# Kernel tuning notes

Measured on AMD Instinct MI355X. Metric: run time of the kernel, lower is better.

The kernel has to match this reference:

```python
import jax, jax.numpy as jnp
import numpy as np

N = 10000      # atoms
E = 64000      # edges (precomputed radius-graph edge list)
B = 128        # molecules in the batch
H = 600        # SCHNET_HIDDEN = num_filters
G = 50         # SCHNET_NUM_GAUSSIANS
L = 6          # SCHNET_NUM_INTERACTIONS
CUTOFF = 10.0  # SCHNET_CUTOFF
ZVOCAB = 100   # PyG SchNet Embedding(100, hidden)
LOG2 = float(np.log(2.0))


def ssp(x):
    # shifted softplus, PyG SchNet activation
    return jax.nn.softplus(x) - LOG2


def setup_inputs() -> dict:
    key = jax.random.key(0)
    ks = jax.random.split(key, 16)
    s_h = 1.0 / np.sqrt(H)
    s_g = 1.0 / np.sqrt(G)
    z = jax.random.randint(ks[0], (N,), 0, 87)
    pos = jax.random.uniform(ks[1], (N, 3), dtype=jnp.float32) * 5.0  # dists < cutoff
    batch = jnp.sort(jax.random.randint(ks[2], (N,), 0, B))
    edge_index = jax.random.randint(ks[3], (2, E), 0, N)
    return {
        'z': z, 'pos': pos, 'batch': batch, 'edge_index': edge_index,
        'emb': jax.random.normal(ks[4], (ZVOCAB, H), jnp.float32) * 0.1,
        'mlp_w1': jax.random.normal(ks[5], (L, G, H), jnp.float32) * s_g,
        'mlp_b1': jnp.zeros((L, H), jnp.float32),
        'mlp_w2': jax.random.normal(ks[6], (L, H, H), jnp.float32) * s_h,
        'mlp_b2': jnp.zeros((L, H), jnp.float32),
        'lin1_w': jax.random.normal(ks[7], (L, H, H), jnp.float32) * s_h,
        'lin2_w': jax.random.normal(ks[8], (L, H, H), jnp.float32) * s_h,
        'lin2_b': jnp.zeros((L, H), jnp.float32),
        'int_lin_w': jax.random.normal(ks[9], (L, H, H), jnp.float32) * s_h,
        'int_lin_b': jnp.zeros((L, H), jnp.float32),
        'pool_w': jax.random.normal(ks[10], (H, H), jnp.float32) * s_h,
        'pool_b': jnp.zeros((H,), jnp.float32),
    }


def reference(z, pos, batch, edge_index, emb,
              mlp_w1, mlp_b1, mlp_w2, mlp_b2,
              lin1_w, lin2_w, lin2_b, int_lin_w, int_lin_b,
              pool_w, pool_b):
    src, dst = edge_index[0], edge_index[1]  # message flows src -> dst
    # edge geometry
    diff = pos[src] - pos[dst]                       # [E,3]
    d = jnp.sqrt(jnp.sum(diff * diff, axis=-1) + 1e-12)  # [E]
    # Gaussian smearing
    offset = jnp.linspace(0.0, CUTOFF, G, dtype=jnp.float32)
    coeff = -0.5 / (offset[1] - offset[0]) ** 2
    rbf = jnp.exp(coeff * (d[:, None] - offset[None, :]) ** 2)  # [E,G]
    # cosine cutoff
    C = 0.5 * (jnp.cos(d * (np.pi / CUTOFF)) + 1.0)             # [E]

    h = emb[z]  # [N,H]
    for k in range(L):
        # per-edge continuous filter
        W = ssp(rbf @ mlp_w1[k] + mlp_b1[k]) @ mlp_w2[k] + mlp_b2[k]  # [E,H]
        W = W * C[:, None]
        # CFConv: project, gather, modulate, scatter-add
        xj = (h @ lin1_w[k])[src]                                     # [E,H]
        agg = jax.ops.segment_sum(xj * W, dst, num_segments=N)        # [N,H]
        x = agg @ lin2_w[k] + lin2_b[k]
        x = ssp(x) @ int_lin_w[k] + int_lin_b[k]
        h = h + x  # residual interaction update

    # per-graph mean pool (segment mean), empty graphs stay zero
    sums = jax.ops.segment_sum(h, batch, num_segments=B)              # [B,H]
    cnt = jax.ops.segment_sum(jnp.ones((h.shape[0],), h.dtype), batch, num_segments=B)
    pooled = sums / jnp.maximum(cnt, 1.0)[:, None]
    return pooled @ pool_w + pool_b
```

## Files before the change

kernel.cpp:

```cpp
#include <hip/hip_runtime.h>
#include <math.h>


#define N_ATOMS 10000
#define E_EDGES 64000
#define B_MOLS  128
#define H_DIM   600
#define HP      608
#define G_DIM   50
#define L_LAYERS 6
#define M_TAB   1024
#define DMAX    8.67f
#define LOG2C   0.69314718056f

#define TM 64
#define TN 64
#define TK 32

typedef __attribute__((ext_vector_type(8))) short bf16x8;
typedef __attribute__((ext_vector_type(4))) float f32x4;

__device__ __forceinline__ float sspf(float x) {
    return fmaxf(x, 0.0f) + log1pf(expf(-fabsf(x))) - LOG2C;
}
__device__ __forceinline__ short f2bf(float x) {
    unsigned u = __float_as_uint(x);
    unsigned r = (u + 0x7FFF + ((u >> 16) & 1)) >> 16;
    return (short)r;
}
__device__ __forceinline__ float bf2f(short h) {
    return __uint_as_float(((unsigned)(unsigned short)h) << 16);
}
__device__ __forceinline__ int packsplit(float x) {
    short hi = f2bf(x);
    short lo = f2bf(x - bf2f(hi));
    return ((int)hi << 16) | ((int)lo & 0xffff);
}
__device__ __forceinline__ float unpackf(int p) {
    float fh = __uint_as_float((unsigned)p & 0xffff0000u);
    float fl = __uint_as_float(((unsigned)p) << 16);
    return fh + fl;
}

__device__ __forceinline__ void unpack_perm(const int4& p0, const int4& p1,
                                            int4& hi, int4& lo)
{
    hi.x = (int)__builtin_amdgcn_perm((unsigned)p0.y, (unsigned)p0.x, 0x07060302u);
    hi.y = (int)__builtin_amdgcn_perm((unsigned)p0.w, (unsigned)p0.z, 0x07060302u);
    hi.z = (int)__builtin_amdgcn_perm((unsigned)p1.y, (unsigned)p1.x, 0x07060302u);
    hi.w = (int)__builtin_amdgcn_perm((unsigned)p1.w, (unsigned)p1.z, 0x07060302u);
    lo.x = (int)__builtin_amdgcn_perm((unsigned)p0.y, (unsigned)p0.x, 0x05040100u);
    lo.y = (int)__builtin_amdgcn_perm((unsigned)p0.w, (unsigned)p0.z, 0x05040100u);
    lo.z = (int)__builtin_amdgcn_perm((unsigned)p1.y, (unsigned)p1.x, 0x05040100u);
    lo.w = (int)__builtin_amdgcn_perm((unsigned)p1.w, (unsigned)p1.z, 0x05040100u);
}

template<bool BIAS, bool ACT, bool ACCUM>
__global__ __launch_bounds__(256, 6)
void gemm_mfma(const int* __restrict__ A, int lda,
               const short* __restrict__ Bh, const short* __restrict__ Bl, int ldb,
               const float* __restrict__ bias,
               int* __restrict__ outP,
               int Ma, int K, int Nc)
{
    const int NT = (Nc + TN - 1) / TN;
    const int f = blockIdx.x;
    const int xcd = f & 7, s = f >> 3;
    const int n0 = (s % NT) * TN;
    const int m0 = (xcd + 8 * (s / NT)) * TM;
    if (m0 >= Ma) return;

    __shared__ __align__(16) short As[2][2048];
    __shared__ __align__(16) short Bs[2][2048];

    const int tid = threadIdx.x;
    const int lane = tid & 63, wid = tid >> 6;
    const int wm = (wid >> 1) * 32, wn = (wid & 1) * 32;
    const int l15 = lane & 15, quad = lane >> 4;

    const int srow = wid * 16 + l15;
    const int skk  = quad << 3;
    const int widx = wid * 512 + lane * 8;

    const int gm = min(m0 + srow, Ma - 1);
    const int gn = min(n0 + srow, Nc - 1);
    const int*   aPtr  = A  + (size_t)gm * lda + skk;
    const short* bPtrH = Bh + (size_t)gn * ldb + skk;
    const short* bPtrL = Bl + (size_t)gn * ldb + skk;

    f32x4 acc[2][2];
    #pragma unroll
    for (int i = 0; i < 2; ++i)
        #pragma unroll
        for (int j = 0; j < 2; ++j)
            acc[i][j] = (f32x4){0.f, 0.f, 0.f, 0.f};

    int4 ra0, ra1;
    bf16x8 rbh, rbl;

    ra0 = *(const int4*)aPtr; ra1 = *(const int4*)(aPtr + 4);
    rbh = *(const bf16x8*)bPtrH;
    rbl = *(const bf16x8*)bPtrL;
    aPtr += TK; bPtrH += TK; bPtrL += TK;

    for (int k0 = 0; k0 < K; k0 += TK) {
        {
            int4 hi, lo;
            unpack_perm(ra0, ra1, hi, lo);
            *(int4*)&As[0][widx] = hi;
            *(int4*)&As[1][widx] = lo;
            *(bf16x8*)&Bs[0][widx] = rbh;
            *(bf16x8*)&Bs[1][widx] = rbl;
        }
        __syncthreads();

        if (k0 + TK < K) {
            ra0 = *(const int4*)aPtr; ra1 = *(const int4*)(aPtr + 4);
            rbh = *(const bf16x8*)bPtrH;
            rbl = *(const bf16x8*)bPtrL;
            aPtr += TK; bPtrH += TK; bPtrL += TK;
        }

        bf16x8 a_h[2], a_l[2], b_h[2], b_l[2];
        #pragma unroll
        for (int mi = 0; mi < 2; ++mi) {
            int ridx = ((wm >> 4) + mi) * 512 + lane * 8;
            a_h[mi] = *(const bf16x8*)&As[0][ridx];
            a_l[mi] = *(const bf16x8*)&As[1][ridx];
        }
        #pragma unroll
        for (int ni = 0; ni < 2; ++ni) {
            int ridx = ((wn >> 4) + ni) * 512 + lane * 8;
            b_h[ni] = *(const bf16x8*)&Bs[0][ridx];
            b_l[ni] = *(const bf16x8*)&Bs[1][ridx];
        }

        #pragma unroll
        for (int mi = 0; mi < 2; ++mi)
            #pragma unroll
            for (int ni = 0; ni < 2; ++ni) {
                acc[mi][ni] = __builtin_amdgcn_mfma_f32_16x16x32_bf16(
                    a_h[mi], b_h[ni], acc[mi][ni], 0, 0, 0);
                acc[mi][ni] = __builtin_amdgcn_mfma_f32_16x16x32_bf16(
                    a_h[mi], b_l[ni], acc[mi][ni], 0, 0, 0);
                acc[mi][ni] = __builtin_amdgcn_mfma_f32_16x16x32_bf16(
                    a_l[mi], b_h[ni], acc[mi][ni], 0, 0, 0);
            }
        __syncthreads();
    }

    #pragma unroll
    for (int mi = 0; mi < 2; ++mi) {
        #pragma unroll
        for (int r = 0; r < 4; ++r) {
            int row = m0 + wm + mi * 16 + quad * 4 + r;
            if (row >= Ma) continue;
            #pragma unroll
            for (int ni = 0; ni < 2; ++ni) {
                int col = n0 + wn + ni * 16 + l15;
                if (col >= HP) continue;
                size_t idx = (size_t)row * HP + col;
                float v = 0.0f;
                if (col < Nc) {
                    v = acc[mi][ni][r];
                    if constexpr (BIAS) v += bias[col];
                    if constexpr (ACT)  v = sspf(v);
                    if constexpr (ACCUM) v += unpackf(outP[idx]);
                }
                outP[idx] = packsplit(v);
            }
        }
    }
}

template<bool SHAREDA, bool ACT>
__global__ __launch_bounds__(256, 6)
void gemm_tab(const int* __restrict__ A, int lda,
              const short* __restrict__ BhBase, const short* __restrict__ BlBase,
              int ldb, int bstride,
              const float* __restrict__ biasBase,
              int* __restrict__ outP,
              int Ma, int K, int Nc)
{
    const int NT = (Nc + TN - 1) / TN;
    const int f = blockIdx.x;
    const int xcd = f & 7, s = f >> 3;
    const int n0 = (s % NT) * TN;
    const int m0 = (xcd + 8 * (s / NT)) * TM;
    if (m0 >= Ma) return;

    const int layer = m0 >> 10;
    const int arow0 = SHAREDA ? (m0 & 1023) : m0;
    const short* __restrict__ Bh = BhBase + (size_t)layer * bstride;
    const short* __restrict__ Bl = BlBase + (size_t)layer * bstride;
    const float* __restrict__ bias = biasBase + (size_t)layer * H_DIM;

    __shared__ __align__(16) short As[2][2048];
    __shared__ __align__(16) short Bs[2][2048];

    const int tid = threadIdx.x;
    const int lane = tid & 63, wid = tid >> 6;
    const int wm = (wid >> 1) * 32, wn = (wid & 1) * 32;
    const int l15 = lane & 15, quad = lane >> 4;

    const int srow = wid * 16 + l15;
    const int skk  = quad << 3;
    const int widx = wid * 512 + lane * 8;

    const int gn = min(n0 + srow, Nc - 1);
    const int*   aPtr  = A  + (size_t)(arow0 + srow) * lda + skk;
    const short* bPtrH = Bh + (size_t)gn * ldb + skk;
    const short* bPtrL = Bl + (size_t)gn * ldb + skk;

    f32x4 acc[2][2];
    #pragma unroll
    for (int i = 0; i < 2; ++i)
        #pragma unroll
        for (int j = 0; j < 2; ++j)
            acc[i][j] = (f32x4){0.f, 0.f, 0.f, 0.f};

    int4 ra0, ra1;
    bf16x8 rbh, rbl;

    ra0 = *(const int4*)aPtr; ra1 = *(const int4*)(aPtr + 4);
    rbh = *(const bf16x8*)bPtrH;
    rbl = *(const bf16x8*)bPtrL;
    aPtr += TK; bPtrH += TK; bPtrL += TK;

    for (int k0 = 0; k0 < K; k0 += TK) {
        {
            int4 hi, lo;
            unpack_perm(ra0, ra1, hi, lo);
            *(int4*)&As[0][widx] = hi;
            *(int4*)&As[1][widx] = lo;
            *(bf16x8*)&Bs[0][widx] = rbh;
            *(bf16x8*)&Bs[1][widx] = rbl;
        }
        __syncthreads();

        if (k0 + TK < K) {
            ra0 = *(const int4*)aPtr; ra1 = *(const int4*)(aPtr + 4);
            rbh = *(const bf16x8*)bPtrH;
            rbl = *(const bf16x8*)bPtrL;
            aPtr += TK; bPtrH += TK; bPtrL += TK;
        }

        bf16x8 a_h[2], a_l[2], b_h[2], b_l[2];
        #pragma unroll
        for (int mi = 0; mi < 2; ++mi) {
            int ridx = ((wm >> 4) + mi) * 512 + lane * 8;
            a_h[mi] = *(const bf16x8*)&As[0][ridx];
            a_l[mi] = *(const bf16x8*)&As[1][ridx];
        }
        #pragma unroll
        for (int ni = 0; ni < 2; ++ni) {
            int ridx = ((wn >> 4) + ni) * 512 + lane * 8;
            b_h[ni] = *(const bf16x8*)&Bs[0][ridx];
            b_l[ni] = *(const bf16x8*)&Bs[1][ridx];
        }
        #pragma unroll
        for (int mi = 0; mi < 2; ++mi)
            #pragma unroll
            for (int ni = 0; ni < 2; ++ni) {
                acc[mi][ni] = __builtin_amdgcn_mfma_f32_16x16x32_bf16(
                    a_h[mi], b_h[ni], acc[mi][ni], 0, 0, 0);
                acc[mi][ni] = __builtin_amdgcn_mfma_f32_16x16x32_bf16(
                    a_h[mi], b_l[ni], acc[mi][ni], 0, 0, 0);
                acc[mi][ni] = __builtin_amdgcn_mfma_f32_16x16x32_bf16(
                    a_l[mi], b_h[ni], acc[mi][ni], 0, 0, 0);
            }
        __syncthreads();
    }

    #pragma unroll
    for (int mi = 0; mi < 2; ++mi) {
        #pragma unroll
        for (int r = 0; r < 4; ++r) {
            int row = m0 + wm + mi * 16 + quad * 4 + r;
            if (row >= Ma) continue;
            #pragma unroll
            for (int ni = 0; ni < 2; ++ni) {
                int col = n0 + wn + ni * 16 + l15;
                if (col >= HP) continue;
                float v = 0.0f;
                if (col < Nc) {
                    v = acc[mi][ni][r] + bias[col];
                    if constexpr (ACT) v = sspf(v);
                }
                outP[(size_t)row * HP + col] = packsplit(v);
            }
        }
    }
}

static inline dim3 mfma_grid(int Ma, int Nc) {
    int MB = (Ma + TM - 1) / TM;
    int NT = (Nc + TN - 1) / TN;
    int Ys = ((MB + 7) / 8) * 8;
    return dim3(Ys * NT);
}

__global__ __launch_bounds__(256)
void pool_mm2_k(const float* __restrict__ A, const float* __restrict__ W,
                const float* __restrict__ bias, float* __restrict__ out)
{
    __shared__ float arow[H_DIM];
    __shared__ float red[4][64];
    const int b = blockIdx.y;
    const int ct = blockIdx.x;
    const int t = threadIdx.x;
    const int ci = t & 63, kq = t >> 6;
    for (int k = t; k < H_DIM; k += 256)
        arow[k] = A[(size_t)b * H_DIM + k];
    __syncthreads();
    const int col = min(ct * 64 + ci, H_DIM - 1);
    const float* wp = W + (size_t)(kq * 150) * H_DIM + col;
    float s = 0.f;
    #pragma unroll 6
    for (int k = 0; k < 150; ++k)
        s = fmaf(arow[kq * 150 + k], wp[(size_t)k * H_DIM], s);
    red[kq][ci] = s;
    __syncthreads();
    if (kq == 0) {
        int c = ct * 64 + ci;
        if (c < H_DIM)
            out[(size_t)b * H_DIM + c] =
                red[0][ci] + red[1][ci] + red[2][ci] + red[3][ci] + bias[c];
    }
}

__global__ __launch_bounds__(256)
void wts_w1_k(const float* __restrict__ w_all, short* __restrict__ oh,
              short* __restrict__ ol)
{
    __shared__ short th[64][65], tl[64][65];
    const int layer = blockIdx.z;
    const float* w = w_all + (size_t)layer * G_DIM * H_DIM;
    short* ohz = oh + (size_t)layer * H_DIM * 64;
    short* olz = ol + (size_t)layer * H_DIM * 64;
    const int n0 = blockIdx.y * 64;
    const int tid = threadIdx.x;
    #pragma unroll
    for (int p = 0; p < 4; ++p) {
        int k = p * 16 + (tid >> 4);
        int n4 = (tid & 15) << 2;
        float4 v = make_float4(0.f, 0.f, 0.f, 0.f);
        if (k < G_DIM && n0 + n4 + 3 < H_DIM)
            v = *(const float4*)(w + (size_t)k * H_DIM + n0 + n4);
        int px = packsplit(v.x), py = packsplit(v.y);
        int pz = packsplit(v.z), pw = packsplit(v.w);
        th[n4 + 0][k] = (short)(px >> 16); tl[n4 + 0][k] = (short)px;
        th[n4 + 1][k] = (short)(py >> 16); tl[n4 + 1][k] = (short)py;
        th[n4 + 2][k] = (short)(pz >> 16); tl[n4 + 2][k] = (short)pz;
        th[n4 + 3][k] = (short)(pw >> 16); tl[n4 + 3][k] = (short)pw;
    }
    __syncthreads();
    #pragma unroll
    for (int p = 0; p < 4; ++p) {
        int n = p * 16 + (tid >> 4);
        int k4 = (tid & 15) << 2;
        if (n0 + n >= H_DIM) continue;
        short4 sh = { th[n][k4], th[n][k4 + 1], th[n][k4 + 2], th[n][k4 + 3] };
        short4 sl = { tl[n][k4], tl[n][k4 + 1], tl[n][k4 + 2], tl[n][k4 + 3] };
        *(short4*)(ohz + (size_t)(n0 + n) * 64 + k4) = sh;
        *(short4*)(olz + (size_t)(n0 + n) * 64 + k4) = sl;
    }
}

__global__ __launch_bounds__(256)
void wts_big_k(const float* __restrict__ w2, const float* __restrict__ l1,
               const float* __restrict__ l2, const float* __restrict__ iw,
               short* __restrict__ oh2, short* __restrict__ ol2,
               short* __restrict__ oh1, short* __restrict__ ol1,
               short* __restrict__ ohl2, short* __restrict__ oll2,
               short* __restrict__ ohi, short* __restrict__ oli)
{
    __shared__ short th[64][65], tl[64][65];
    const int z = blockIdx.z, type = z / L_LAYERS, layer = z % L_LAYERS;
    const float* w; short* oh; short* ol;
    if (type == 0)      { w = w2; oh = oh2; ol = ol2; }
    else if (type == 1) { w = l1; oh = oh1; ol = ol1; }
    else if (type == 2) { w = l2; oh = ohl2; ol = oll2; }
    else                { w = iw; oh = ohi; ol = oli; }
    w  += (size_t)layer * H_DIM * H_DIM;
    oh += (size_t)layer * H_DIM * HP;
    ol += (size_t)layer * H_DIM * HP;
    const int k0 = blockIdx.x * 64, n0 = blockIdx.y * 64;
    const int tid = threadIdx.x;
    #pragma unroll
    for (int p = 0; p < 4; ++p) {
        int k = p * 16 + (tid >> 4);
        int n4 = (tid & 15) << 2;
        float4 v = make_float4(0.f, 0.f, 0.f, 0.f);
        if (k0 + k < H_DIM && n0 + n4 + 3 < H_DIM)
            v = *(const float4*)(w + (size_t)(k0 + k) * H_DIM + n0 + n4);
        int px = packsplit(v.x), py = packsplit(v.y);
        int pz = packsplit(v.z), pw = packsplit(v.w);
        th[n4 + 0][k] = (short)(px >> 16); tl[n4 + 0][k] = (short)px;
        th[n4 + 1][k] = (short)(py >> 16); tl[n4 + 1][k] = (short)py;
        th[n4 + 2][k] = (short)(pz >> 16); tl[n4 + 2][k] = (short)pz;
        th[n4 + 3][k] = (short)(pw >> 16); tl[n4 + 3][k] = (short)pw;
    }
    __syncthreads();
    #pragma unroll
    for (int p = 0; p < 4; ++p) {
        int n = p * 16 + (tid >> 4);
        int k4 = (tid & 15) << 2;
        if (n0 + n >= H_DIM || k0 + k4 > HP - 4) continue;
        short4 sh = { th[n][k4], th[n][k4 + 1], th[n][k4 + 2], th[n][k4 + 3] };
        short4 sl = { tl[n][k4], tl[n][k4 + 1], tl[n][k4 + 2], tl[n][k4 + 3] };
        *(short4*)(oh + (size_t)(n0 + n) * HP + k0 + k4) = sh;
        *(short4*)(ol + (size_t)(n0 + n) * HP + k0 + k4) = sl;
    }
}

__global__ __launch_bounds__(256)
void init_h_k(const int* __restrict__ z, const float* __restrict__ emb,
              int* __restrict__ hP)
{
    int t = blockIdx.x * 256 + threadIdx.x;
    const int QC = HP / 4;
    if (t >= N_ATOMS * QC) return;
    int i = t / QC;
    int q = (t - i * QC) << 2;
    size_t idx = (size_t)i * HP + q;
    if (q < H_DIM) {
        float4 v = *(const float4*)(emb + (size_t)z[i] * H_DIM + q);
        *(int4*)(hP + idx) = make_int4(packsplit(v.x), packsplit(v.y),
                                       packsplit(v.z), packsplit(v.w));
    } else {
        *(int4*)(hP + idx) = make_int4(0, 0, 0, 0);
    }
}

__global__ __launch_bounds__(256)
void edge_geom_k(const float* __restrict__ pos, const int* __restrict__ src,
                 const int* __restrict__ dst, float4* __restrict__ einfo)
{
    int e = blockIdx.x * 256 + threadIdx.x;
    if (e >= E_EDGES) return;
    int s = src[e], d0 = dst[e];
    float dx = pos[s * 3 + 0] - pos[d0 * 3 + 0];
    float dy = pos[s * 3 + 1] - pos[d0 * 3 + 1];
    float dz = pos[s * 3 + 2] - pos[d0 * 3 + 2];
    float dist = sqrtf(dx * dx + dy * dy + dz * dz + 1e-12f);
    float cc = 0.5f * (cosf(dist * 0.31415926535f) + 1.0f);
    float u = dist * ((float)(M_TAB - 1) / DMAX);
    u = fminf(fmaxf(u, 0.0f), (float)(M_TAB - 1) - 0.001f);
    int i0 = (int)u;
    float fc = (u - (float)i0) * cc;
    einfo[e] = make_float4(__int_as_float(s * HP),
                           __int_as_float(i0 * HP),
                           cc - fc, fc);
}

__global__ __launch_bounds__(256)
void rbf_tab_k(int* __restrict__ rtabP)
{
    int t = blockIdx.x * 256 + threadIdx.x;
    if (t >= M_TAB * 64) return;
    int i = t >> 6, g = t & 63;
    float v = 0.0f;
    if (g < G_DIM) {
        float dg  = (float)i * (DMAX / (float)(M_TAB - 1));
        float off = (float)g * (10.0f / 49.0f);
        float x = dg - off;
        const float coeff = -0.5f * (49.0f / 10.0f) * (49.0f / 10.0f);
        v = expf(coeff * x * x);
    }
    rtabP[t] = packsplit(v);
}

__global__ __launch_bounds__(256)
void hist_k(const int* __restrict__ dst, int* __restrict__ deg)
{
    int e = blockIdx.x * 256 + threadIdx.x;
    if (e >= E_EDGES) return;
    atomicAdd(&deg[dst[e]], 1);
}

__global__ __launch_bounds__(1024)
void scan_k(const int* __restrict__ deg, int* __restrict__ rowptr)
{
    __shared__ int sums[1024];
    int tid = threadIdx.x;
    const int CHUNK = (N_ATOMS + 1023) / 1024;
    int base = tid * CHUNK;
    int local[16];
    int s = 0;
    #pragma unroll
    for (int c = 0; c < 16; ++c) {
        if (c >= CHUNK) break;
        int idx = base + c;
        local[c] = s;
        s += (idx < N_ATOMS) ? deg[idx] : 0;
    }
    sums[tid] = s;
    __syncthreads();
    for (int off = 1; off < 1024; off <<= 1) {
        int v = (tid >= off) ? sums[tid - off] : 0;
        __syncthreads();
        sums[tid] += v;
        __syncthreads();
    }
    int prefix = (tid > 0) ? sums[tid - 1] : 0;
    #pragma unroll
    for (int c = 0; c < 16; ++c) {
        if (c >= CHUNK) break;
        int idx = base + c;
        if (idx <= N_ATOMS) rowptr[idx] = prefix + local[c];
    }
    if (tid == 1023) rowptr[N_ATOMS] = sums[1023];
}

__global__ __launch_bounds__(256)
void fill_k(const int* __restrict__ dst, const float4* __restrict__ einfo,
            const int* __restrict__ rowptr, int* __restrict__ cursor,
            float4* __restrict__ esorted)
{
    int e = blockIdx.x * 256 + threadIdx.x;
    if (e >= E_EDGES) return;
    int d0 = dst[e];
    int pos = rowptr[d0] + atomicAdd(&cursor[d0], 1);
    esorted[pos] = einfo[e];
}

__global__ __launch_bounds__(256)
void bounds_k(const int* __restrict__ batch, int* __restrict__ mrow)
{
    int b = threadIdx.x;
    if (b > B_MOLS) return;
    int lo = 0, hi = N_ATOMS;
    while (lo < hi) {
        int mid = (lo + hi) >> 1;
        if (batch[mid] < b) lo = mid + 1; else hi = mid;
    }
    mrow[b] = lo;
}

__device__ __forceinline__ void gacc(float4& acc, const int* yP, const int* wtP,
                                     const float4& ei, int q)
{
    int srow = __float_as_int(ei.x);
    int wrow = __float_as_int(ei.y);
    float a = ei.z, b = ei.w;
    int4 yv = *(const int4*)(yP + srow + q);
    int4 w0 = *(const int4*)(wtP + wrow + q);
    int4 w1 = *(const int4*)(wtP + wrow + HP + q);
    acc.x += unpackf(yv.x) * (a * unpackf(w0.x) + b * unpackf(w1.x));
    acc.y += unpackf(yv.y) * (a * unpackf(w0.y) + b * unpackf(w1.y));
    acc.z += unpackf(yv.z) * (a * unpackf(w0.z) + b * unpackf(w1.z));
    acc.w += unpackf(yv.w) * (a * unpackf(w0.w) + b * unpackf(w1.w));
}

__global__ __launch_bounds__(256)
void gather_k(const int* __restrict__ yP, const int* __restrict__ wtP,
              const int* __restrict__ rowptr, const float4* __restrict__ esorted,
              int* __restrict__ aggP)
{
    int t = blockIdx.x * 256 + threadIdx.x;
    const int QC = HP / 4;
    if (t >= N_ATOMS * QC) return;
    int i = t / QC;
    int q = (t - i * QC) << 2;
    size_t idx = (size_t)i * HP + q;
    if (q >= H_DIM) { *(int4*)(aggP + idx) = make_int4(0, 0, 0, 0); return; }
    int j0 = rowptr[i], j1 = rowptr[i + 1];
    float4 a0 = make_float4(0.f, 0.f, 0.f, 0.f);
    float4 a1 = make_float4(0.f, 0.f, 0.f, 0.f);
    int j = j0;
    for (; j + 2 <= j1; j += 2) {
        float4 e0 = esorted[j], e1 = esorted[j + 1];
        gacc(a0, yP, wtP, e0, q);
        gacc(a1, yP, wtP, e1, q);
    }
    if (j < j1) gacc(a0, yP, wtP, esorted[j], q);
    a0.x += a1.x; a0.y += a1.y; a0.z += a1.z; a0.w += a1.w;
    *(int4*)(aggP + idx) = make_int4(packsplit(a0.x), packsplit(a0.y),
                                     packsplit(a0.z), packsplit(a0.w));
}

__global__ __launch_bounds__(256)
void pool_seg_k(const int* __restrict__ hP, const int* __restrict__ mrow,
                float* __restrict__ pooled)
{
    int b = blockIdx.x;
    int t = threadIdx.x;
    if (t >= 150) return;
    int q = t << 2;
    int a = mrow[b], a1 = mrow[b + 1];
    float cnt = (float)(a1 - a);
    float4 s0 = make_float4(0.f, 0.f, 0.f, 0.f);
    float4 s1 = make_float4(0.f, 0.f, 0.f, 0.f);
    for (; a + 2 <= a1; a += 2) {
        int4 p0 = *(const int4*)(hP + (size_t)a * HP + q);
        int4 p1 = *(const int4*)(hP + (size_t)(a + 1) * HP + q);
        s0.x += unpackf(p0.x); s0.y += unpackf(p0.y);
        s0.z += unpackf(p0.z); s0.w += unpackf(p0.w);
        s1.x += unpackf(p1.x); s1.y += unpackf(p1.y);
        s1.z += unpackf(p1.z); s1.w += unpackf(p1.w);
    }
    if (a < a1) {
        int4 p0 = *(const int4*)(hP + (size_t)a * HP + q);
        s0.x += unpackf(p0.x); s0.y += unpackf(p0.y);
        s0.z += unpackf(p0.z); s0.w += unpackf(p0.w);
    }
    float inv = 1.0f / fmaxf(cnt, 1.0f);
    float4 o = make_float4((s0.x + s1.x) * inv, (s0.y + s1.y) * inv,
                           (s0.z + s1.z) * inv, (s0.w + s1.w) * inv);
    *(float4*)(pooled + (size_t)b * H_DIM + q) = o;
}

extern "C" void kernel_launch(void* const* d_in, const int* in_sizes, int n_in,
                              void* d_out, int out_size, void* d_ws, size_t ws_size,
                              hipStream_t stream)
{
    const int*   z      = (const int*)  d_in[0];
    const float* pos    = (const float*)d_in[1];
    const int*   batch  = (const int*)  d_in[2];
    const int*   eidx   = (const int*)  d_in[3];
    const float* emb    = (const float*)d_in[4];
    const float* mlp_w1 = (const float*)d_in[5];
    const float* mlp_b1 = (const float*)d_in[6];
    const float* mlp_w2 = (const float*)d_in[7];
    const float* mlp_b2 = (const float*)d_in[8];
    const float* lin1_w = (const float*)d_in[9];
    const float* lin2_w = (const float*)d_in[10];
    const float* lin2_b = (const float*)d_in[11];
    const float* intw   = (const float*)d_in[12];
    const float* intb   = (const float*)d_in[13];
    const float* poolw  = (const float*)d_in[14];
    const float* poolb  = (const float*)d_in[15];

    float* ws = (float*)d_ws;
    const size_t NHP = (size_t)N_ATOMS * HP;
    const size_t TABALL = (size_t)L_LAYERS * M_TAB * HP;

    int*   hP    = (int*)ws;
    int*   y1P   = (int*)(ws + NHP);
    int*   tP    = y1P;
    int*   ttabA = y1P;
    int*   aggP  = (int*)(ws + 2 * NHP);
    float4* einfo  = (float4*)aggP;
    int*    deg    = (int*)((float*)aggP + 300000);
    int*    cursor = (int*)((float*)aggP + 310000);
    int*   wtabA = (int*)(ws + 3 * NHP);
    int*   rtabP = (int*)(ws + 3 * NHP + TABALL);
    short* wtH   = (short*)(ws + 3 * NHP + TABALL + (size_t)M_TAB * 64);
    short* wtL   = wtH + 8985600;
    float*  tailF   = (float*)(wtL + 8985600);
    float4* esorted = (float4*)tailF;
    float*  pooled  = tailF + 256000;
    int*    rowptr  = (int*)(tailF + 332800);
    int*    mrow    = rowptr + 10001;

    short* w1t_h = wtH;                       short* w1t_l = wtL;
    short* w2t_h = wtH + 230400;              short* w2t_l = wtL + 230400;
    short* l1t_h = w2t_h + 6 * 600 * HP;      short* l1t_l = w2t_l + 6 * 600 * HP;
    short* l2t_h = l1t_h + 6 * 600 * HP;      short* l2t_l = l1t_l + 6 * 600 * HP;
    short* int_h = l2t_h + 6 * 600 * HP;      short* int_l = l2t_l + 6 * 600 * HP;

    const int* src = eidx;
    const int* dst = eidx + E_EDGES;

    const dim3 blk(256);
    const int QC = HP / 4;
    const dim3 gN   = mfma_grid(N_ATOMS, H_DIM);
    const dim3 gTab = mfma_grid(L_LAYERS * M_TAB, H_DIM);

    edge_geom_k<<<(E_EDGES + 255) / 256, blk, 0, stream>>>(pos, src, dst, einfo);
    hipMemsetAsync(deg, 0, 2 * N_ATOMS * sizeof(int), stream);
    hist_k <<<(E_EDGES + 255) / 256, blk, 0, stream>>>(dst, deg);
    scan_k <<<1, 1024, 0, stream>>>(deg, rowptr);
    fill_k <<<(E_EDGES + 255) / 256, blk, 0, stream>>>(dst, einfo, rowptr, cursor, esorted);
    bounds_k <<<1, 256, 0, stream>>>(batch, mrow);
    init_h_k <<<(N_ATOMS * QC + 255) / 256, blk, 0, stream>>>(z, emb, hP);
    rbf_tab_k<<<(M_TAB * 64 + 255) / 256,   blk, 0, stream>>>(rtabP);
    wts_w1_k  <<<dim3(1, 10, 6),   blk, 0, stream>>>(mlp_w1, w1t_h, w1t_l);
    wts_big_k <<<dim3(10, 10, 24), blk, 0, stream>>>(
        mlp_w2, lin1_w, lin2_w, intw,
        w2t_h, w2t_l, l1t_h, l1t_l, l2t_h, l2t_l, int_h, int_l);

    gemm_tab<true, true><<<gTab, blk, 0, stream>>>(
        rtabP, 64, w1t_h, w1t_l, 64, 600 * 64, mlp_b1,
        ttabA, L_LAYERS * M_TAB, 64, H_DIM);
    gemm_tab<false, false><<<gTab, blk, 0, stream>>>(
        ttabA, HP, w2t_h, w2t_l, HP, 600 * HP, mlp_b2,
        wtabA, L_LAYERS * M_TAB, HP, H_DIM);

    for (int k = 0; k < L_LAYERS; ++k) {
        const float* l2b = lin2_b + (size_t)k * H_DIM;
        const float* ib  = intb   + (size_t)k * H_DIM;
        const short* l1h = l1t_h + (size_t)k * H_DIM * HP;
        const short* l1l = l1t_l + (size_t)k * H_DIM * HP;
        const short* l2h = l2t_h + (size_t)k * H_DIM * HP;
        const short* l2l = l2t_l + (size_t)k * H_DIM * HP;
        const short* ih  = int_h + (size_t)k * H_DIM * HP;
        const short* il  = int_l + (size_t)k * H_DIM * HP;
        const int*   wtP = wtabA + (size_t)k * M_TAB * HP;

        gemm_mfma<false, false, false><<<gN, blk, 0, stream>>>(
            hP, HP, l1h, l1l, HP, nullptr, y1P, N_ATOMS, HP, H_DIM);
        gather_k<<<(N_ATOMS * QC + 255) / 256, blk, 0, stream>>>(
            y1P, wtP, rowptr, esorted, aggP);
        gemm_mfma<true, true, false><<<gN, blk, 0, stream>>>(
            aggP, HP, l2h, l2l, HP, l2b, tP, N_ATOMS, HP, H_DIM);
        gemm_mfma<true, false, true><<<gN, blk, 0, stream>>>(
            tP, HP, ih, il, HP, ib, hP, N_ATOMS, HP, H_DIM);
    }

    pool_seg_k<<<B_MOLS, blk, 0, stream>>>(hP, mrow, pooled);
    pool_mm2_k<<<dim3(10, B_MOLS), blk, 0, stream>>>(
        pooled, poolw, poolb, (float*)d_out);
}
```

Baseline: 1.443 ms.

## Pre-tile split-bf16 weights into MFMA fragment order and pad A shared tile

Weight preprocessing now writes the hi/lo bf16 halves into contiguous 4096-element tiles laid out in the exact MFMA fragment order, so each GEMM thread loads its B fragment with one fully coalesced vector load per tile instead of strided row reads from two separate arrays. The A operand is now loaded row-major with a padded shared-memory stride (40 shorts) so global reads are contiguous per row and LDS fragment reads avoid bank conflicts. The W1 tile buffer moves into scratch space inside the aggregation region. This relies on that region's lifetime not overlapping other uses, and it changes the indexing of every GEMM.

```diff
diff --git a/kernel.cpp b/kernel.cpp
--- a/kernel.cpp
+++ b/kernel.cpp
@@ -16,6 +16,14 @@
 #define TM 64
 #define TN 64
 #define TK 32
+#define SA 40
+
+#define BTILE 4096
+#define NTILES_H 10
+#define KT_BIG 19
+#define KT_W1  2
+#define BSTRIDE_BIG (NTILES_H * KT_BIG * BTILE)
+#define BSTRIDE_W1  (NTILES_H * KT_W1  * BTILE)
 
 typedef __attribute__((ext_vector_type(8))) short bf16x8;
 typedef __attribute__((ext_vector_type(4))) float f32x4;
@@ -58,7 +66,7 @@
 template<bool BIAS, bool ACT, bool ACCUM>
 __global__ __launch_bounds__(256, 6)
 void gemm_mfma(const int* __restrict__ A, int lda,
-               const short* __restrict__ Bh, const short* __restrict__ Bl, int ldb,
+               const short* __restrict__ Bt,
                const float* __restrict__ bias,
                int* __restrict__ outP,
                int Ma, int K, int Nc)
@@ -69,24 +77,21 @@
     const int n0 = (s % NT) * TN;
     const int m0 = (xcd + 8 * (s / NT)) * TM;
     if (m0 >= Ma) return;
-
-    __shared__ __align__(16) short As[2][2048];
+    const int KT = (K + 31) >> 5;
+
+    __shared__ __align__(16) short As[2][TM * SA];
     __shared__ __align__(16) short Bs[2][2048];
 
     const int tid = threadIdx.x;
     const int lane = tid & 63, wid = tid >> 6;
     const int wm = (wid >> 1) * 32, wn = (wid & 1) * 32;
     const int l15 = lane & 15, quad = lane >> 4;
-
-    const int srow = wid * 16 + l15;
-    const int skk  = quad << 3;
-    const int widx = wid * 512 + lane * 8;
+    const int srow = tid >> 2;
+    const int skk  = (tid & 3) << 3;
 
     const int gm = min(m0 + srow, Ma - 1);
-    const int gn = min(n0 + srow, Nc - 1);
-    const int*   aPtr  = A  + (size_t)gm * lda + skk;
-    const short* bPtrH = Bh + (size_t)gn * ldb + skk;
-    const short* bPtrL = Bl + (size_t)gn * ldb + skk;
+    const int*   aPtr = A + (size_t)gm * lda + skk;
+    const short* bPtr = Bt + ((size_t)(n0 >> 6) * KT) * BTILE + tid * 8;
 
     f32x4 acc[2][2];
     #pragma unroll
@@ -99,34 +104,34 @@
     bf16x8 rbh, rbl;
 
     ra0 = *(const int4*)aPtr; ra1 = *(const int4*)(aPtr + 4);
-    rbh = *(const bf16x8*)bPtrH;
-    rbl = *(const bf16x8*)bPtrL;
-    aPtr += TK; bPtrH += TK; bPtrL += TK;
+    rbh = *(const bf16x8*)bPtr;
+    rbl = *(const bf16x8*)(bPtr + 2048);
+    aPtr += TK; bPtr += BTILE;
 
     for (int k0 = 0; k0 < K; k0 += TK) {
         {
             int4 hi, lo;
             unpack_perm(ra0, ra1, hi, lo);
-            *(int4*)&As[0][widx] = hi;
-            *(int4*)&As[1][widx] = lo;
-            *(bf16x8*)&Bs[0][widx] = rbh;
-            *(bf16x8*)&Bs[1][widx] = rbl;
+            *(int4*)&As[0][srow * SA + skk] = hi;
+            *(int4*)&As[1][srow * SA + skk] = lo;
+            *(bf16x8*)&Bs[0][tid * 8] = rbh;
+            *(bf16x8*)&Bs[1][tid * 8] = rbl;
         }
         __syncthreads();
 
         if (k0 + TK < K) {
             ra0 = *(const int4*)aPtr; ra1 = *(const int4*)(aPtr + 4);
-            rbh = *(const bf16x8*)bPtrH;
-            rbl = *(const bf16x8*)bPtrL;
-            aPtr += TK; bPtrH += TK; bPtrL += TK;
+            rbh = *(const bf16x8*)bPtr;
+            rbl = *(const bf16x8*)(bPtr + 2048);
+            aPtr += TK; bPtr += BTILE;
         }
 
         bf16x8 a_h[2], a_l[2], b_h[2], b_l[2];
         #pragma unroll
         for (int mi = 0; mi < 2; ++mi) {
-            int ridx = ((wm >> 4) + mi) * 512 + lane * 8;
-            a_h[mi] = *(const bf16x8*)&As[0][ridx];
-            a_l[mi] = *(const bf16x8*)&As[1][ridx];
+            int row = wm + mi * 16 + l15;
+            a_h[mi] = *(const bf16x8*)&As[0][row * SA + quad * 8];
+            a_l[mi] = *(const bf16x8*)&As[1][row * SA + quad * 8];
         }
         #pragma unroll
         for (int ni = 0; ni < 2; ++ni) {
@@ -176,8 +181,7 @@
 template<bool SHAREDA, bool ACT>
 __global__ __launch_bounds__(256, 6)
 void gemm_tab(const int* __restrict__ A, int lda,
-              const short* __restrict__ BhBase, const short* __restrict__ BlBase,
-              int ldb, int bstride,
+              const short* __restrict__ BtBase, size_t bstride,
               const float* __restrict__ biasBase,
               int* __restrict__ outP,
               int Ma, int K, int Nc)
@@ -188,29 +192,25 @@
     const int n0 = (s % NT) * TN;
     const int m0 = (xcd + 8 * (s / NT)) * TM;
     if (m0 >= Ma) return;
+    const int KT = (K + 31) >> 5;
 
     const int layer = m0 >> 10;
     const int arow0 = SHAREDA ? (m0 & 1023) : m0;
-    const short* __restrict__ Bh = BhBase + (size_t)layer * bstride;
-    const short* __restrict__ Bl = BlBase + (size_t)layer * bstride;
+    const short* __restrict__ Bt = BtBase + (size_t)layer * bstride;
     const float* __restrict__ bias = biasBase + (size_t)layer * H_DIM;
 
-    __shared__ __align__(16) short As[2][2048];
+    __shared__ __align__(16) short As[2][TM * SA];
     __shared__ __align__(16) short Bs[2][2048];
 
     const int tid = threadIdx.x;
     const int lane = tid & 63, wid = tid >> 6;
     const int wm = (wid >> 1) * 32, wn = (wid & 1) * 32;
     const int l15 = lane & 15, quad = lane >> 4;
-
-    const int srow = wid * 16 + l15;
-    const int skk  = quad << 3;
-    const int widx = wid * 512 + lane * 8;
-
-    const int gn = min(n0 + srow, Nc - 1);
-    const int*   aPtr  = A  + (size_t)(arow0 + srow) * lda + skk;
-    const short* bPtrH = Bh + (size_t)gn * ldb + skk;
-    const short* bPtrL = Bl + (size_t)gn * ldb + skk;
+    const int srow = tid >> 2;
+    const int skk  = (tid & 3) << 3;
+
+    const int*   aPtr = A + (size_t)(arow0 + srow) * lda + skk;
+    const short* bPtr = Bt + ((size_t)(n0 >> 6) * KT) * BTILE + tid * 8;
 
     f32x4 acc[2][2];
     #pragma unroll
@@ -223,34 +223,34 @@
     bf16x8 rbh, rbl;
 
     ra0 = *(const int4*)aPtr; ra1 = *(const int4*)(aPtr + 4);
-    rbh = *(const bf16x8*)bPtrH;
-    rbl = *(const bf16x8*)bPtrL;
-    aPtr += TK; bPtrH += TK; bPtrL += TK;
+    rbh = *(const bf16x8*)bPtr;
+    rbl = *(const bf16x8*)(bPtr + 2048);
+    aPtr += TK; bPtr += BTILE;
 
     for (int k0 = 0; k0 < K; k0 += TK) {
         {
             int4 hi, lo;
             unpack_perm(ra0, ra1, hi, lo);
-            *(int4*)&As[0][widx] = hi;
-            *(int4*)&As[1][widx] = lo;
-            *(bf16x8*)&Bs[0][widx] = rbh;
-            *(bf16x8*)&Bs[1][widx] = rbl;
+            *(int4*)&As[0][srow * SA + skk] = hi;
+            *(int4*)&As[1][srow * SA + skk] = lo;
+            *(bf16x8*)&Bs[0][tid * 8] = rbh;
+            *(bf16x8*)&Bs[1][tid * 8] = rbl;
         }
         __syncthreads();
 
         if (k0 + TK < K) {
             ra0 = *(const int4*)aPtr; ra1 = *(const int4*)(aPtr + 4);
-            rbh = *(const bf16x8*)bPtrH;
-            rbl = *(const bf16x8*)bPtrL;
-            aPtr += TK; bPtrH += TK; bPtrL += TK;
+            rbh = *(const bf16x8*)bPtr;
+            rbl = *(const bf16x8*)(bPtr + 2048);
+            aPtr += TK; bPtr += BTILE;
         }
 
         bf16x8 a_h[2], a_l[2], b_h[2], b_l[2];
         #pragma unroll
         for (int mi = 0; mi < 2; ++mi) {
-            int ridx = ((wm >> 4) + mi) * 512 + lane * 8;
-            a_h[mi] = *(const bf16x8*)&As[0][ridx];
-            a_l[mi] = *(const bf16x8*)&As[1][ridx];
+            int row = wm + mi * 16 + l15;
+            a_h[mi] = *(const bf16x8*)&As[0][row * SA + quad * 8];
+            a_l[mi] = *(const bf16x8*)&As[1][row * SA + quad * 8];
         }
         #pragma unroll
         for (int ni = 0; ni < 2; ++ni) {
@@ -330,15 +330,14 @@
 }
 
 __global__ __launch_bounds__(256)
-void wts_w1_k(const float* __restrict__ w_all, short* __restrict__ oh,
-              short* __restrict__ ol)
+void wts_w1_k(const float* __restrict__ w_all, short* __restrict__ w1t)
 {
     __shared__ short th[64][65], tl[64][65];
     const int layer = blockIdx.z;
+    const int nt = blockIdx.y;
     const float* w = w_all + (size_t)layer * G_DIM * H_DIM;
-    short* ohz = oh + (size_t)layer * H_DIM * 64;
-    short* olz = ol + (size_t)layer * H_DIM * 64;
-    const int n0 = blockIdx.y * 64;
+    short* outb = w1t + (size_t)layer * BSTRIDE_W1 + (size_t)nt * KT_W1 * BTILE;
+    const int n0 = nt * 64;
     const int tid = threadIdx.x;
     #pragma unroll
     for (int p = 0; p < 4; ++p) {
@@ -359,33 +358,32 @@
     for (int p = 0; p < 4; ++p) {
         int n = p * 16 + (tid >> 4);
         int k4 = (tid & 15) << 2;
-        if (n0 + n >= H_DIM) continue;
+        int kt = k4 >> 5, kk = k4 & 31;
+        int idx = (n >> 4) * 512 + (kk >> 3) * 128 + (n & 15) * 8 + (kk & 7);
+        short* tb = outb + (size_t)kt * BTILE;
         short4 sh = { th[n][k4], th[n][k4 + 1], th[n][k4 + 2], th[n][k4 + 3] };
         short4 sl = { tl[n][k4], tl[n][k4 + 1], tl[n][k4 + 2], tl[n][k4 + 3] };
-        *(short4*)(ohz + (size_t)(n0 + n) * 64 + k4) = sh;
-        *(short4*)(olz + (size_t)(n0 + n) * 64 + k4) = sl;
+        *(short4*)(tb + idx)        = sh;
+        *(short4*)(tb + 2048 + idx) = sl;
     }
 }
 
 __global__ __launch_bounds__(256)
 void wts_big_k(const float* __restrict__ w2, const float* __restrict__ l1,
                const float* __restrict__ l2, const float* __restrict__ iw,
-               short* __restrict__ oh2, short* __restrict__ ol2,
-               short* __restrict__ oh1, short* __restrict__ ol1,
-               short* __restrict__ ohl2, short* __restrict__ oll2,
-               short* __restrict__ ohi, short* __restrict__ oli)
+               short* __restrict__ o2, short* __restrict__ o1,
+               short* __restrict__ ol2, short* __restrict__ oi)
 {
     __shared__ short th[64][65], tl[64][65];
     const int z = blockIdx.z, type = z / L_LAYERS, layer = z % L_LAYERS;
-    const float* w; short* oh; short* ol;
-    if (type == 0)      { w = w2; oh = oh2; ol = ol2; }
-    else if (type == 1) { w = l1; oh = oh1; ol = ol1; }
-    else if (type == 2) { w = l2; oh = ohl2; ol = oll2; }
-    else                { w = iw; oh = ohi; ol = oli; }
+    const float* w; short* ob;
+    if (type == 0)      { w = w2; ob = o2; }
+    else if (type == 1) { w = l1; ob = o1; }
+    else if (type == 2) { w = l2; ob = ol2; }
+    else                { w = iw; ob = oi; }
     w  += (size_t)layer * H_DIM * H_DIM;
-    oh += (size_t)layer * H_DIM * HP;
-    ol += (size_t)layer * H_DIM * HP;
-    const int k0 = blockIdx.x * 64, n0 = blockIdx.y * 64;
+    ob += (size_t)layer * BSTRIDE_BIG;
+    const int k0 = blockIdx.x * 64, nt = blockIdx.y, n0 = nt * 64;
     const int tid = threadIdx.x;
     #pragma unroll
     for (int p = 0; p < 4; ++p) {
@@ -406,11 +404,15 @@
     for (int p = 0; p < 4; ++p) {
         int n = p * 16 + (tid >> 4);
         int k4 = (tid & 15) << 2;
-        if (n0 + n >= H_DIM || k0 + k4 > HP - 4) continue;
+        int kg = k0 + k4;
+        if (kg >= KT_BIG * 32) continue;
+        int kt = kg >> 5, kk = kg & 31;
+        int idx = (n >> 4) * 512 + (kk >> 3) * 128 + (n & 15) * 8 + (kk & 7);
+        short* tb = ob + ((size_t)nt * KT_BIG + kt) * BTILE;
         short4 sh = { th[n][k4], th[n][k4 + 1], th[n][k4 + 2], th[n][k4 + 3] };
         short4 sl = { tl[n][k4], tl[n][k4 + 1], tl[n][k4 + 2], tl[n][k4 + 3] };
-        *(short4*)(oh + (size_t)(n0 + n) * HP + k0 + k4) = sh;
-        *(short4*)(ol + (size_t)(n0 + n) * HP + k0 + k4) = sl;
+        *(short4*)(tb + idx)        = sh;
+        *(short4*)(tb + 2048 + idx) = sl;
     }
 }
 
@@ -644,21 +646,19 @@
     float4* einfo  = (float4*)aggP;
     int*    deg    = (int*)((float*)aggP + 300000);
     int*    cursor = (int*)((float*)aggP + 310000);
+    short*  w1t    = (short*)((float*)aggP + 400000);
     int*   wtabA = (int*)(ws + 3 * NHP);
     int*   rtabP = (int*)(ws + 3 * NHP + TABALL);
-    short* wtH   = (short*)(ws + 3 * NHP + TABALL + (size_t)M_TAB * 64);
-    short* wtL   = wtH + 8985600;
-    float*  tailF   = (float*)(wtL + 8985600);
+    short* wtT   = (short*)(ws + 3 * NHP + TABALL + (size_t)M_TAB * 64);
+    short* w2t = wtT;
+    short* l1t = w2t + (size_t)L_LAYERS * BSTRIDE_BIG;
+    short* l2t = l1t + (size_t)L_LAYERS * BSTRIDE_BIG;
+    short* itt = l2t + (size_t)L_LAYERS * BSTRIDE_BIG;
+    float*  tailF   = (float*)(itt + (size_t)L_LAYERS * BSTRIDE_BIG);
     float4* esorted = (float4*)tailF;
     float*  pooled  = tailF + 256000;
     int*    rowptr  = (int*)(tailF + 332800);
     int*    mrow    = rowptr + 10001;
-
-    short* w1t_h = wtH;                       short* w1t_l = wtL;
-    short* w2t_h = wtH + 230400;              short* w2t_l = wtL + 230400;
-    short* l1t_h = w2t_h + 6 * 600 * HP;      short* l1t_l = w2t_l + 6 * 600 * HP;
-    short* l2t_h = l1t_h + 6 * 600 * HP;      short* l2t_l = l1t_l + 6 * 600 * HP;
-    short* int_h = l2t_h + 6 * 600 * HP;      short* int_l = l2t_l + 6 * 600 * HP;
 
     const int* src = eidx;
     const int* dst = eidx + E_EDGES;
@@ -676,37 +676,33 @@
     bounds_k <<<1, 256, 0, stream>>>(batch, mrow);
     init_h_k <<<(N_ATOMS * QC + 255) / 256, blk, 0, stream>>>(z, emb, hP);
     rbf_tab_k<<<(M_TAB * 64 + 255) / 256,   blk, 0, stream>>>(rtabP);
-    wts_w1_k  <<<dim3(1, 10, 6),   blk, 0, stream>>>(mlp_w1, w1t_h, w1t_l);
+    wts_w1_k  <<<dim3(1, 10, 6),   blk, 0, stream>>>(mlp_w1, w1t);
     wts_big_k <<<dim3(10, 10, 24), blk, 0, stream>>>(
-        mlp_w2, lin1_w, lin2_w, intw,
-        w2t_h, w2t_l, l1t_h, l1t_l, l2t_h, l2t_l, int_h, int_l);
+        mlp_w2, lin1_w, lin2_w, intw, w2t, l1t, l2t, itt);
 
     gemm_tab<true, true><<<gTab, blk, 0, stream>>>(
-        rtabP, 64, w1t_h, w1t_l, 64, 600 * 64, mlp_b1,
+        rtabP, 64, w1t, (size_t)BSTRIDE_W1, mlp_b1,
         ttabA, L_LAYERS * M_TAB, 64, H_DIM);
     gemm_tab<false, false><<<gTab, blk, 0, stream>>>(
-        ttabA, HP, w2t_h, w2t_l, HP, 600 * HP, mlp_b2,
+        ttabA, HP, w2t, (size_t)BSTRIDE_BIG, mlp_b2,
         wtabA, L_LAYERS * M_TAB, HP, H_DIM);
 
     for (int k = 0; k < L_LAYERS; ++k) {
         const float* l2b = lin2_b + (size_t)k * H_DIM;
         const float* ib  = intb   + (size_t)k * H_DIM;
-        const short* l1h = l1t_h + (size_t)k * H_DIM * HP;
-        const short* l1l = l1t_l + (size_t)k * H_DIM * HP;
-        const short* l2h = l2t_h + (size_t)k * H_DIM * HP;
-        const short* l2l = l2t_l + (size_t)k * H_DIM * HP;
-        const short* ih  = int_h + (size_t)k * H_DIM * HP;
-        const short* il  = int_l + (size_t)k * H_DIM * HP;
+        const short* l1 = l1t + (size_t)k * BSTRIDE_BIG;
+        const short* l2 = l2t + (size_t)k * BSTRIDE_BIG;
+        const short* it = itt + (size_t)k * BSTRIDE_BIG;
         const int*   wtP = wtabA + (size_t)k * M_TAB * HP;
 
         gemm_mfma<false, false, false><<<gN, blk, 0, stream>>>(
-            hP, HP, l1h, l1l, HP, nullptr, y1P, N_ATOMS, HP, H_DIM);
+            hP, HP, l1, nullptr, y1P, N_ATOMS, HP, H_DIM);
         gather_k<<<(N_ATOMS * QC + 255) / 256, blk, 0, stream>>>(
             y1P, wtP, rowptr, esorted, aggP);
         gemm_mfma<true, true, false><<<gN, blk, 0, stream>>>(
-            aggP, HP, l2h, l2l, HP, l2b, tP, N_ATOMS, HP, H_DIM);
+            aggP, HP, l2, l2b, tP, N_ATOMS, HP, H_DIM);
         gemm_mfma<true, false, true><<<gN, blk, 0, stream>>>(
-            tP, HP, ih, il, HP, ib, hP, N_ATOMS, HP, H_DIM);
+            tP, HP, it, ib, hP, N_ATOMS, HP, H_DIM);
     }
 
     pool_seg_k<<<B_MOLS, blk, 0, stream>>>(hP, mrow, pooled);
```

After: 1.213 ms. 1.19x faster.
